# Kernel tuning notes

Hardware: AMD Instinct MI355X
Metric: run time of the kernel (lower is better)

The kernel has to match this reference:

```python
import jax, jax.numpy as jnp
import numpy as np

HEAD_NUM = 16
D_MODEL = 1024
D_K = D_MODEL // HEAD_NUM


def setup_inputs() -> dict:
    key = jax.random.key(0)
    ks = jax.random.split(key, 11)
    B, S = 2, 2048
    scale = 1.0 / np.sqrt(D_MODEL)
    inp = {
        'query': jax.random.normal(ks[0], (B, S, D_MODEL), jnp.float32),
        'key': jax.random.normal(ks[1], (B, S, D_MODEL), jnp.float32),
        'value': jax.random.normal(ks[2], (B, S, D_MODEL), jnp.float32),
        'W1': jax.random.normal(ks[3], (D_MODEL, D_MODEL), jnp.float32) * scale,
        'b1': jax.random.normal(ks[4], (D_MODEL,), jnp.float32) * 0.02,
        'W2': jax.random.normal(ks[5], (D_MODEL, D_MODEL), jnp.float32) * scale,
        'b2': jax.random.normal(ks[6], (D_MODEL,), jnp.float32) * 0.02,
        'W3': jax.random.normal(ks[7], (D_MODEL, D_MODEL), jnp.float32) * scale,
        'b3': jax.random.normal(ks[8], (D_MODEL,), jnp.float32) * 0.02,
        'W4': jax.random.normal(ks[9], (D_MODEL, D_MODEL), jnp.float32) * scale,
        'b4': jax.random.normal(ks[10], (D_MODEL,), jnp.float32) * 0.02,
    }
    return inp


def reference(query, key, value, W1, b1, W2, b2, W3, b3, W4, b4):
    B, S, _ = query.shape
    # linear projections (torch Linear: x @ W^T + b)
    q = query @ W1.T + b1
    k = key @ W2.T + b2
    v = value @ W3.T + b3
    # [B, H, S, d_k]
    q = q.reshape(B, S, HEAD_NUM, D_K).transpose(0, 2, 1, 3)
    k = k.reshape(B, S, HEAD_NUM, D_K).transpose(0, 2, 1, 3)
    v = v.reshape(B, S, HEAD_NUM, D_K).transpose(0, 2, 1, 3)
    # scaled dot-product attention
    scores = jnp.einsum('bhqd,bhkd->bhqk', q, k) / np.sqrt(D_K).astype(jnp.float32)
    attn = jax.nn.softmax(scores, axis=-1)
    out = jnp.einsum('bhqk,bhkd->bhqd', attn, v)
    # merge heads -> [B, S, d_model]
    out = out.transpose(0, 2, 1, 3).reshape(B, S, D_MODEL)
    result = out @ W4.T + b4
    return result
```

## Files before the change

kernel.cpp:

```cpp
#include <hip/hip_runtime.h>
#include <hip/hip_bf16.h>
#include <stdint.h>

typedef unsigned short u16;
typedef unsigned int   u32;
typedef __attribute__((ext_vector_type(4))) float f32x4;
typedef __attribute__((ext_vector_type(8))) short bf16x8;

__device__ __forceinline__ u16 f2bf(float x){
  u32 u = __float_as_uint(x);
  return (u16)((u + 0x7fffu + ((u >> 16) & 1u)) >> 16);
}

__device__ __forceinline__ u32 pkbf(float a, float b){
  __hip_bfloat162 t = __float22bfloat162_rn(make_float2(a, b));
  u32 r; __builtin_memcpy(&r, &t, 4); return r;
}

__device__ __forceinline__ float fexp2(float x){
  float r; asm("v_exp_f32 %0, %1" : "=v"(r) : "v"(x)); return r;
}

__device__ __forceinline__ void pl16swap(u32 &d, u32 &s){
  asm("v_permlane16_swap_b32 %0, %1" : "+v"(d), "+v"(s));
}

__device__ __forceinline__ bf16x8 mk8(u32 a, u32 b, u32 c, u32 d){
  union { u32 w[4]; bf16x8 v; } t; t.w[0]=a; t.w[1]=b; t.w[2]=c; t.w[3]=d; return t.v;
}

__device__ __forceinline__ void async_cp16(const void* g, void* l){
  __builtin_amdgcn_global_load_lds((const __attribute__((address_space(1))) void*)g,
                                   (__attribute__((address_space(3))) void*)l, 16, 0, 0);
}

__device__ __forceinline__ void conv_body(const float* __restrict__ x,
                                          u16* __restrict__ hi, int i){
  float4 v = *(const float4*)(x + i);
  ushort4 hv; hv.x = f2bf(v.x); hv.y = f2bf(v.y); hv.z = f2bf(v.z); hv.w = f2bf(v.w);
  *(ushort4*)(hi + i) = hv;
}

__global__ __launch_bounds__(256) void conv_all(
    const float* __restrict__ q, const float* __restrict__ k, const float* __restrict__ v,
    const float* __restrict__ w1, const float* __restrict__ w2,
    const float* __restrict__ w3, const float* __restrict__ w4,
    u16* qh, u16* kh, u16* vh, u16* w1h, u16* w2h, u16* w3h, u16* w4h)
{
  const int o = blockIdx.x;
  const float* x; u16* y; int blk;
  if (o < 12288){
    const int z = o >> 12;
    blk = o & 4095;
    x = (z == 0) ? q : (z == 1) ? k : v;
    y = (z == 0) ? qh : (z == 1) ? kh : vh;
  } else {
    const int o2 = o - 12288;
    const int z = o2 >> 10;
    blk = o2 & 1023;
    x = (z == 0) ? w1 : (z == 1) ? w2 : (z == 2) ? w3 : w4;
    y = (z == 0) ? w1h : (z == 1) ? w2h : (z == 2) ? w3h : w4h;
  }
  conv_body(x, y, (blk * 256 + threadIdx.x) * 4);
}

template<int OUT>
__device__ __forceinline__ void gemm_plain(
    const u16* __restrict__ A, const u16* __restrict__ B,
    const float* __restrict__ bias, void* __restrict__ outp, float scale, int m0, int n0)
{
  __shared__ u16 lA[8192], lB[8192];
  const int tid  = threadIdx.x;
  const int lane = tid & 63, wid = tid >> 6;
  const int li = lane & 15, g = lane >> 4;
  const int wr = wid >> 1, wc = wid & 1;

  const u16* pA = A + (size_t)m0 * 1024;
  const u16* pB = B + (size_t)n0 * 1024;

  const int r0 = tid >> 3, c0 = tid & 7;
  const size_t gsrc = (size_t)r0 * 1024 + (size_t)((c0 ^ (r0 & 7)) * 8);
  char* dA = (char*)lA + wid * 1024;
  char* dB = (char*)lB + wid * 1024;

  f32x4 acc[4][4];
  #pragma unroll
  for (int i = 0; i < 4; i++)
    #pragma unroll
    for (int j = 0; j < 4; j++) acc[i][j] = (f32x4){0.f, 0.f, 0.f, 0.f};

  for (int k0 = 0; k0 < 1024; k0 += 64){
    __syncthreads();
    #pragma unroll
    for (int s = 0; s < 4; s++){
      async_cp16(pA + gsrc + k0 + (size_t)s * 32 * 1024, dA + s * 4096);
      async_cp16(pB + gsrc + k0 + (size_t)s * 32 * 1024, dB + s * 4096);
    }
    __syncthreads();

    #pragma unroll
    for (int kk = 0; kk < 2; kk++){
      bf16x8 af[4], bf4[4];
      #pragma unroll
      for (int f = 0; f < 4; f++){
        int ar = wr * 64 + f * 16 + li;
        int ja = (kk * 4 + g) ^ (ar & 7);
        af[f] = *(const bf16x8*)((const char*)lA + ar * 128 + (ja << 4));
        int br = wc * 64 + f * 16 + li;
        int jb = (kk * 4 + g) ^ (br & 7);
        bf4[f] = *(const bf16x8*)((const char*)lB + br * 128 + (jb << 4));
      }
      __builtin_amdgcn_s_setprio(1);
      #pragma unroll
      for (int fm = 0; fm < 4; fm++)
        #pragma unroll
        for (int fn = 0; fn < 4; fn++)
          acc[fm][fn] = __builtin_amdgcn_mfma_f32_16x16x32_bf16(af[fm], bf4[fn], acc[fm][fn], 0, 0, 0);
      __builtin_amdgcn_s_setprio(0);
    }
  }

  float bv[4];
  #pragma unroll
  for (int fn = 0; fn < 4; fn++) bv[fn] = bias[n0 + wc * 64 + fn * 16 + li];

  #pragma unroll
  for (int fm = 0; fm < 4; fm++){
    const int mb = m0 + wr * 64 + fm * 16 + g * 4;
    #pragma unroll
    for (int fn = 0; fn < 4; fn++){
      const int n = n0 + wc * 64 + fn * 16 + li;
      #pragma unroll
      for (int r = 0; r < 4; r++){
        float v = acc[fm][fn][r] + bv[fn];
        if (OUT == 0) ((u16*)outp)[(size_t)(mb + r) * 1024 + n] = f2bf(v * scale);
        else          ((float*)outp)[(size_t)(mb + r) * 1024 + n] = v;
      }
    }
  }
}

__global__ __launch_bounds__(256, 2) void proj_kernel(
    const u16* qh, const u16* kh, const u16* vh,
    const u16* w1h, const u16* w2h, const u16* w3h,
    const float* b1, const float* b2, const float* b3,
    u16* Qb, u16* Kb, u16* Vb)
{
  const int o = blockIdx.x;
  const int swz = (o & 7) * 96 + (o >> 3);
  const int x = swz & 7, y = (swz >> 3) & 31, z = swz >> 8;
  const u16 *A, *B; const float* bs; u16* out; float sc;
  if (z == 0){ A = qh; B = w1h; bs = b1; out = Qb; sc = 0.18033688011112042f; }
  else if (z == 1){ A = kh; B = w2h; bs = b2; out = Kb; sc = 1.0f; }
  else { A = vh; B = w3h; bs = b3; out = Vb; sc = 1.0f; }
  gemm_plain<0>(A, B, bs, out, sc, y * 128, x * 128);
}

__global__ __launch_bounds__(256, 2) void fin_kernel(
    const u16* __restrict__ A, const u16* __restrict__ B,
    const float* __restrict__ bias, float* __restrict__ out)
{
  const int o = blockIdx.x;
  const int swz = (o & 7) * 32 + (o >> 3);
  const int x = swz & 7, y = swz >> 3;
  gemm_plain<1>(A, B, bias, out, 1.0f, y * 128, x * 128);
}

__global__ __launch_bounds__(256) void transpose_v(const u16* __restrict__ Vb, u16* __restrict__ VbT){
  __shared__ u16 T[64][72];
  const int t = threadIdx.x;
  const int kt = blockIdx.x, h = blockIdx.y, b = blockIdx.z;
  const int r = t >> 2, c0 = (t & 3) * 16;
  const u16* src = Vb + (size_t)(b * 2048 + kt * 64 + r) * 1024 + h * 64 + c0;
  *(bf16x8*)&T[r][c0]     = *(const bf16x8*)(src);
  *(bf16x8*)&T[r][c0 + 8] = *(const bf16x8*)(src + 8);
  __syncthreads();
  const int d = t >> 2, kc = (t & 3) * 16;
  bf16x8 o0, o1;
  #pragma unroll
  for (int j = 0; j < 8; j++){ o0[j] = (short)T[kc + j][d]; o1[j] = (short)T[kc + 8 + j][d]; }
  u16* dst = VbT + ((size_t)(b * 16 + h) * 64 + d) * 2048 + kt * 64 + kc;
  *(bf16x8*)dst       = o0;
  *(bf16x8*)(dst + 8) = o1;
}

__global__ __launch_bounds__(256) void attn_kernel(
    const u16* __restrict__ Qb, const u16* __restrict__ Kb, const u16* __restrict__ VbT,
    u16* __restrict__ AOh)
{
  __shared__ u16 KT[2][8192];
  __shared__ u16 VT[2][8192];
  char* Kc = (char*)KT; char* Vc = (char*)VT;

  const int tid = threadIdx.x;
  const int lane = tid & 63, wid = tid >> 6;
  const int li = lane & 15, g = lane >> 4;

  const int o = blockIdx.x;
  const int swz = (o & 7) * 64 + (o >> 3);
  const int qt = swz & 15, h = (swz >> 4) & 15, b = swz >> 8;

  const int r0 = tid >> 3, ch = tid & 7;
  const int cswz8 = (ch ^ (r0 & 7)) * 8;
  const u16* gK = Kb + (size_t)(b * 2048 + r0) * 1024 + h * 64 + cswz8;
  const int vr = tid >> 4, vc = tid & 15;
  const int vsw = (vc ^ (vr & 7)) * 8;
  const u16* gV = VbT + ((size_t)(b * 16 + h) * 64 + vr) * 2048 + vsw;
  const int ldsB = wid * 1024;

  const int kb0 = li * 128 + ((g ^ (li & 7)) << 4);
  const int cm = ((((g & 1) << 1) | ((g >> 1) & 1)) ^ 2);
  const int lx = li & 7;
  const int vc0 = ((cm ^ lx) << 4);
  const int vc1 = (((4 + cm) ^ lx) << 4);
  const int vrb = li * 256;

  const u16* qp = Qb + (size_t)(b * 2048 + qt * 128 + wid * 32 + li) * 1024 + h * 64 + g * 8;
  bf16x8 qf[2][2];
  qf[0][0] = *(const bf16x8*)(qp);
  qf[0][1] = *(const bf16x8*)(qp + 32);
  qf[1][0] = *(const bf16x8*)(qp + 16 * 1024);
  qf[1][1] = *(const bf16x8*)(qp + 16 * 1024 + 32);

  f32x4 O[2][4];
  #pragma unroll
  for (int st = 0; st < 2; st++)
    #pragma unroll
    for (int df = 0; df < 4; df++) O[st][df] = (f32x4){0.f, 0.f, 0.f, 0.f};
  f32x4 Lacc[2];
  Lacc[0] = (f32x4){0.f, 0.f, 0.f, 0.f};
  Lacc[1] = (f32x4){0.f, 0.f, 0.f, 0.f};
  const f32x4 NEGC = (f32x4){-32.f, -32.f, -32.f, -32.f};
  const u32 one2 = 0x3f803f80u;
  const bf16x8 ones = mk8(one2, one2, one2, one2);

  #pragma unroll
  for (int s = 0; s < 4; s++){
    async_cp16(gK + s * 32768, Kc + ldsB + s * 4096);
    async_cp16(gV + s * 32768, Vc + ldsB + s * 4096);
  }

  int cur = 0;
  for (int t = 0; t < 16; t++){
    if (t < 15){
      const int kn = (t + 1) * 128;
      const int nb = (cur ^ 1) * 16384;
      #pragma unroll
      for (int s = 0; s < 4; s++){
        async_cp16(gK + (size_t)kn * 1024 + s * 32768, Kc + nb + ldsB + s * 4096);
        async_cp16(gV + kn + s * 32768,                Vc + nb + ldsB + s * 4096);
      }
      asm volatile("s_waitcnt vmcnt(8)" ::: "memory");
    } else {
      asm volatile("s_waitcnt vmcnt(0)" ::: "memory");
    }
    __builtin_amdgcn_sched_barrier(0);
    __builtin_amdgcn_s_barrier();
    __builtin_amdgcn_sched_barrier(0);

    const char* Kb_ = Kc + cur * 16384;
    const char* Vb_ = Vc + cur * 16384;

    f32x4 scA[2][4], scB[2][4];
    __builtin_amdgcn_s_setprio(1);
    #pragma unroll
    for (int fn = 0; fn < 4; fn++){
      bf16x8 kf0 = *(const bf16x8*)(Kb_ + fn * 2048 + kb0);
      bf16x8 kf1 = *(const bf16x8*)(Kb_ + fn * 2048 + (kb0 ^ 64));
      #pragma unroll
      for (int st = 0; st < 2; st++){
        f32x4 z = __builtin_amdgcn_mfma_f32_16x16x32_bf16(kf0, qf[st][0], NEGC, 0, 0, 0);
        scA[st][fn] = __builtin_amdgcn_mfma_f32_16x16x32_bf16(kf1, qf[st][1], z, 0, 0, 0);
      }
    }
    #pragma unroll
    for (int fn = 0; fn < 4; fn++){
      bf16x8 kf0 = *(const bf16x8*)(Kb_ + 8192 + fn * 2048 + kb0);
      bf16x8 kf1 = *(const bf16x8*)(Kb_ + 8192 + fn * 2048 + (kb0 ^ 64));
      #pragma unroll
      for (int st = 0; st < 2; st++){
        f32x4 z = __builtin_amdgcn_mfma_f32_16x16x32_bf16(kf0, qf[st][0], NEGC, 0, 0, 0);
        scB[st][fn] = __builtin_amdgcn_mfma_f32_16x16x32_bf16(kf1, qf[st][1], z, 0, 0, 0);
      }
    }
    __builtin_amdgcn_s_setprio(0);

    #pragma unroll
    for (int kt = 0; kt < 2; kt++){
      bf16x8 pa[2][2];
      #pragma unroll
      for (int st = 0; st < 2; st++){
        float p[4][4];
        #pragma unroll
        for (int fn = 0; fn < 4; fn++)
          #pragma unroll
          for (int r = 0; r < 4; r++)
            p[fn][r] = fexp2(kt == 0 ? scA[st][fn][r] : scB[st][fn][r]);

        #pragma unroll
        for (int ks = 0; ks < 2; ks++){
          u32 a0 = pkbf(p[2 * ks][0],     p[2 * ks][1]);
          u32 a1 = pkbf(p[2 * ks][2],     p[2 * ks][3]);
          u32 b0 = pkbf(p[2 * ks + 1][0], p[2 * ks + 1][1]);
          u32 b1 = pkbf(p[2 * ks + 1][2], p[2 * ks + 1][3]);
          pl16swap(b0, a0);
          pl16swap(b1, a1);
          pa[st][ks] = mk8(b0, b1, a0, a1);
        }
      }

      __builtin_amdgcn_s_setprio(1);
      #pragma unroll
      for (int ks = 0; ks < 2; ks++){
        Lacc[0] = __builtin_amdgcn_mfma_f32_16x16x32_bf16(ones, pa[0][ks], Lacc[0], 0, 0, 0);
        Lacc[1] = __builtin_amdgcn_mfma_f32_16x16x32_bf16(ones, pa[1][ks], Lacc[1], 0, 0, 0);
        #pragma unroll
        for (int df = 0; df < 4; df++){
          bf16x8 vf = *(const bf16x8*)(Vb_ + df * 4096 + vrb + kt * 128 + (ks ? vc1 : vc0));
          O[0][df] = __builtin_amdgcn_mfma_f32_16x16x32_bf16(vf, pa[0][ks], O[0][df], 0, 0, 0);
          O[1][df] = __builtin_amdgcn_mfma_f32_16x16x32_bf16(vf, pa[1][ks], O[1][df], 0, 0, 0);
        }
      }
      __builtin_amdgcn_s_setprio(0);
    }

    __builtin_amdgcn_sched_barrier(0);
    __builtin_amdgcn_s_barrier();
    cur ^= 1;
  }

  const int rowb = b * 2048 + qt * 128 + wid * 32;
  #pragma unroll
  for (int st = 0; st < 2; st++){
    const float inv = 1.0f / Lacc[st][0];
    #pragma unroll
    for (int df = 0; df < 4; df++){
      ushort4 hv;
      #pragma unroll
      for (int r = 0; r < 4; r++)
        ((u16*)&hv)[r] = f2bf(O[st][df][r] * inv);
      size_t idx = (size_t)(rowb + st * 16 + li) * 1024 + h * 64 + df * 16 + g * 4;
      *(ushort4*)(AOh + idx) = hv;
    }
  }
}

extern "C" void kernel_launch(void* const* d_in, const int* in_sizes, int n_in,
                              void* d_out, int out_size, void* d_ws, size_t ws_size,
                              hipStream_t stream)
{
  (void)in_sizes; (void)n_in; (void)out_size; (void)ws_size;
  const float* query = (const float*)d_in[0];
  const float* key_  = (const float*)d_in[1];
  const float* value = (const float*)d_in[2];
  const float* W1 = (const float*)d_in[3];
  const float* b1 = (const float*)d_in[4];
  const float* W2 = (const float*)d_in[5];
  const float* b2 = (const float*)d_in[6];
  const float* W3 = (const float*)d_in[7];
  const float* b3 = (const float*)d_in[8];
  const float* W4 = (const float*)d_in[9];
  const float* b4 = (const float*)d_in[10];

  char* w = (char*)d_ws;
  const size_t MB = (size_t)1 << 20;
  u16* qh  = (u16*)(w +  0 * MB);
  u16* kh  = (u16*)(w +  8 * MB);
  u16* vh  = (u16*)(w + 16 * MB);
  u16* w1h = (u16*)(w + 24 * MB);
  u16* w2h = (u16*)(w + 26 * MB);
  u16* w3h = (u16*)(w + 28 * MB);
  u16* w4h = (u16*)(w + 30 * MB);
  u16* Qb  = (u16*)(w + 32 * MB);
  u16* Kb  = (u16*)(w + 40 * MB);
  u16* Vb  = (u16*)(w + 48 * MB);
  u16* VbT = (u16*)(w + 56 * MB);
  u16* AOh = (u16*)(w + 64 * MB);

  conv_all<<<16384, 256, 0, stream>>>(query, key_, value, W1, W2, W3, W4,
                                      qh, kh, vh, w1h, w2h, w3h, w4h);

  proj_kernel<<<768, 256, 0, stream>>>(qh, kh, vh, w1h, w2h, w3h, b1, b2, b3, Qb, Kb, Vb);
  transpose_v<<<dim3(32, 16, 2), 256, 0, stream>>>(Vb, VbT);
  attn_kernel<<<512, 256, 0, stream>>>(Qb, Kb, VbT, AOh);
  fin_kernel<<<256, 256, 0, stream>>>(AOh, w4h, b4, (float*)d_out);
}
```

Baseline: 125.6 us.

## Fuse fp32-to-bf16 activation conversion into projection GEMM A-tile loading

The separate conversion pass over query, key and value is dropped. The projection kernel now loads fp32 activations straight into registers, packs them to bf16 and writes them to swizzled LDS, while weight tiles arrive through double-buffered async copies. This removes one full read and write of the 48 MB of activations plus the bf16 re-read. In exchange, each projection block reads fp32 A tiles (twice the bytes), and across the eight column blocks that re-read can cost global bandwidth and register pressure.

After: 119.7 us. 1.05x faster.

```diff
diff --git a/kernel.cpp b/kernel.cpp
--- a/kernel.cpp
+++ b/kernel.cpp
@@ -42,25 +42,15 @@
 }
 
 __global__ __launch_bounds__(256) void conv_all(
-    const float* __restrict__ q, const float* __restrict__ k, const float* __restrict__ v,
     const float* __restrict__ w1, const float* __restrict__ w2,
     const float* __restrict__ w3, const float* __restrict__ w4,
-    u16* qh, u16* kh, u16* vh, u16* w1h, u16* w2h, u16* w3h, u16* w4h)
+    u16* w1h, u16* w2h, u16* w3h, u16* w4h)
 {
   const int o = blockIdx.x;
-  const float* x; u16* y; int blk;
-  if (o < 12288){
-    const int z = o >> 12;
-    blk = o & 4095;
-    x = (z == 0) ? q : (z == 1) ? k : v;
-    y = (z == 0) ? qh : (z == 1) ? kh : vh;
-  } else {
-    const int o2 = o - 12288;
-    const int z = o2 >> 10;
-    blk = o2 & 1023;
-    x = (z == 0) ? w1 : (z == 1) ? w2 : (z == 2) ? w3 : w4;
-    y = (z == 0) ? w1h : (z == 1) ? w2h : (z == 2) ? w3h : w4h;
-  }
+  const int z = o >> 10;
+  const int blk = o & 1023;
+  const float* x = (z == 0) ? w1 : (z == 1) ? w2 : (z == 2) ? w3 : w4;
+  u16* y = (z == 0) ? w1h : (z == 1) ? w2h : (z == 2) ? w3h : w4h;
   conv_body(x, y, (blk * 256 + threadIdx.x) * 4);
 }
 
@@ -141,19 +131,124 @@
 }
 
 __global__ __launch_bounds__(256, 2) void proj_kernel(
-    const u16* qh, const u16* kh, const u16* vh,
-    const u16* w1h, const u16* w2h, const u16* w3h,
+    const float* __restrict__ qf, const float* __restrict__ kf, const float* __restrict__ vf,
+    const u16* __restrict__ w1h, const u16* __restrict__ w2h, const u16* __restrict__ w3h,
     const float* b1, const float* b2, const float* b3,
     u16* Qb, u16* Kb, u16* Vb)
 {
+  __shared__ u16 lA[8192];
+  __shared__ u16 lB[2][8192];
+
   const int o = blockIdx.x;
   const int swz = (o & 7) * 96 + (o >> 3);
   const int x = swz & 7, y = (swz >> 3) & 31, z = swz >> 8;
-  const u16 *A, *B; const float* bs; u16* out; float sc;
-  if (z == 0){ A = qh; B = w1h; bs = b1; out = Qb; sc = 0.18033688011112042f; }
-  else if (z == 1){ A = kh; B = w2h; bs = b2; out = Kb; sc = 1.0f; }
-  else { A = vh; B = w3h; bs = b3; out = Vb; sc = 1.0f; }
-  gemm_plain<0>(A, B, bs, out, sc, y * 128, x * 128);
+  const float* Af; const u16* Bw; const float* bs; u16* out; float sc;
+  if (z == 0){ Af = qf; Bw = w1h; bs = b1; out = Qb; sc = 0.18033688011112042f; }
+  else if (z == 1){ Af = kf; Bw = w2h; bs = b2; out = Kb; sc = 1.0f; }
+  else { Af = vf; Bw = w3h; bs = b3; out = Vb; sc = 1.0f; }
+
+  const int tid  = threadIdx.x;
+  const int lane = tid & 63, wid = tid >> 6;
+  const int li = lane & 15, g = lane >> 4;
+  const int wr = wid >> 1, wc = wid & 1;
+  const int m0 = y * 128, n0 = x * 128;
+
+  const int r0 = tid >> 3, c0 = tid & 7;
+  const size_t gsB = (size_t)r0 * 1024 + (size_t)((c0 ^ (r0 & 7)) * 8);
+  const u16* pB = Bw + (size_t)n0 * 1024;
+
+  const int ar0 = wid * 32 + (lane >> 3);
+  const int ac  = lane & 7;
+  const int awb = ((ac ^ (lane >> 3)) << 4);
+  const float* pA = Af + (size_t)m0 * 1024;
+
+  float4 ap[4][2];
+  auto loadA = [&](int k0){
+    #pragma unroll
+    for (int p = 0; p < 4; p++){
+      const float* s = pA + (size_t)(ar0 + 8 * p) * 1024 + k0 + ac * 8;
+      ap[p][0] = *(const float4*)s;
+      ap[p][1] = *(const float4*)(s + 4);
+    }
+  };
+
+  f32x4 acc[4][4];
+  #pragma unroll
+  for (int i = 0; i < 4; i++)
+    #pragma unroll
+    for (int j = 0; j < 4; j++) acc[i][j] = (f32x4){0.f, 0.f, 0.f, 0.f};
+
+  loadA(0);
+  #pragma unroll
+  for (int s = 0; s < 4; s++)
+    async_cp16(pB + gsB + (size_t)s * 32 * 1024, (char*)lB + wid * 1024 + s * 4096);
+
+  int cur = 0;
+  for (int t = 0; t < 16; t++){
+    const int k0 = t * 64;
+    __builtin_amdgcn_s_barrier();
+    asm volatile("s_waitcnt vmcnt(0)" ::: "memory");
+    __builtin_amdgcn_sched_barrier(0);
+
+    #pragma unroll
+    for (int p = 0; p < 4; p++){
+      uint4 wv;
+      wv.x = pkbf(ap[p][0].x, ap[p][0].y);
+      wv.y = pkbf(ap[p][0].z, ap[p][0].w);
+      wv.z = pkbf(ap[p][1].x, ap[p][1].y);
+      wv.w = pkbf(ap[p][1].z, ap[p][1].w);
+      *(uint4*)((char*)lA + (ar0 + 8 * p) * 128 + awb) = wv;
+    }
+    if (t < 15){
+      loadA(k0 + 64);
+      #pragma unroll
+      for (int s = 0; s < 4; s++)
+        async_cp16(pB + gsB + (k0 + 64) + (size_t)s * 32 * 1024,
+                   (char*)lB + (cur ^ 1) * 16384 + wid * 1024 + s * 4096);
+    }
+    asm volatile("s_waitcnt lgkmcnt(0)" ::: "memory");
+    __builtin_amdgcn_sched_barrier(0);
+    __builtin_amdgcn_s_barrier();
+
+    const char* Bb = (const char*)lB + cur * 16384;
+    #pragma unroll
+    for (int kk = 0; kk < 2; kk++){
+      bf16x8 af[4], bf4[4];
+      #pragma unroll
+      for (int f = 0; f < 4; f++){
+        int ar = wr * 64 + f * 16 + li;
+        int ja = (kk * 4 + g) ^ (ar & 7);
+        af[f] = *(const bf16x8*)((const char*)lA + ar * 128 + (ja << 4));
+        int br = wc * 64 + f * 16 + li;
+        int jb = (kk * 4 + g) ^ (br & 7);
+        bf4[f] = *(const bf16x8*)(Bb + br * 128 + (jb << 4));
+      }
+      __builtin_amdgcn_s_setprio(1);
+      #pragma unroll
+      for (int fm = 0; fm < 4; fm++)
+        #pragma unroll
+        for (int fn = 0; fn < 4; fn++)
+          acc[fm][fn] = __builtin_amdgcn_mfma_f32_16x16x32_bf16(af[fm], bf4[fn], acc[fm][fn], 0, 0, 0);
+      __builtin_amdgcn_s_setprio(0);
+    }
+    cur ^= 1;
+  }
+
+  float bv[4];
+  #pragma unroll
+  for (int fn = 0; fn < 4; fn++) bv[fn] = bs[n0 + wc * 64 + fn * 16 + li];
+
+  #pragma unroll
+  for (int fm = 0; fm < 4; fm++){
+    const int mb = m0 + wr * 64 + fm * 16 + g * 4;
+    #pragma unroll
+    for (int fn = 0; fn < 4; fn++){
+      const int n = n0 + wc * 64 + fn * 16 + li;
+      #pragma unroll
+      for (int r = 0; r < 4; r++)
+        out[(size_t)(mb + r) * 1024 + n] = f2bf((acc[fm][fn][r] + bv[fn]) * sc);
+    }
+  }
 }
 
 __global__ __launch_bounds__(256, 2) void fin_kernel(
@@ -364,9 +459,6 @@
 
   char* w = (char*)d_ws;
   const size_t MB = (size_t)1 << 20;
-  u16* qh  = (u16*)(w +  0 * MB);
-  u16* kh  = (u16*)(w +  8 * MB);
-  u16* vh  = (u16*)(w + 16 * MB);
   u16* w1h = (u16*)(w + 24 * MB);
   u16* w2h = (u16*)(w + 26 * MB);
   u16* w3h = (u16*)(w + 28 * MB);
@@ -377,10 +469,10 @@
   u16* VbT = (u16*)(w + 56 * MB);
   u16* AOh = (u16*)(w + 64 * MB);
 
-  conv_all<<<16384, 256, 0, stream>>>(query, key_, value, W1, W2, W3, W4,
-                                      qh, kh, vh, w1h, w2h, w3h, w4h);
-
-  proj_kernel<<<768, 256, 0, stream>>>(qh, kh, vh, w1h, w2h, w3h, b1, b2, b3, Qb, Kb, Vb);
+  conv_all<<<4096, 256, 0, stream>>>(W1, W2, W3, W4, w1h, w2h, w3h, w4h);
+
+  proj_kernel<<<768, 256, 0, stream>>>(query, key_, value, w1h, w2h, w3h,
+                                       b1, b2, b3, Qb, Kb, Vb);
   transpose_v<<<dim3(32, 16, 2), 256, 0, stream>>>(Vb, VbT);
   attn_kernel<<<512, 256, 0, stream>>>(Qb, Kb, VbT, AOh);
   fin_kernel<<<256, 256, 0, stream>>>(AOh, w4h, b4, (float*)d_out);
```
